# Optimization experiments

Measured on AMD Instinct MI355X. Metric: run time of the kernel, lower is better.

The kernel has to match this reference:

```python
import jax, jax.numpy as jnp
import numpy as np


def setup_inputs() -> dict:
    key = jax.random.key(0)
    ks = jax.random.split(key, 9)
    B, C, H, W = 16, 64, 64, 64
    s = 0.02
    return {
        "x": jax.random.normal(ks[0], (B, C, H, W), dtype=jnp.float32),
        "qw": jax.random.normal(ks[1], (C, C), dtype=jnp.float32) * s,
        "qb": jax.random.normal(ks[2], (C,), dtype=jnp.float32) * s,
        "kw": jax.random.normal(ks[3], (C, C), dtype=jnp.float32) * s,
        "kb": jax.random.normal(ks[4], (C,), dtype=jnp.float32) * s,
        "vw": jax.random.normal(ks[5], (C, C), dtype=jnp.float32) * s,
        "vb": jax.random.normal(ks[6], (C,), dtype=jnp.float32) * s,
        "ow": jax.random.normal(ks[7], (C, C), dtype=jnp.float32) * s,
        "ob": jax.random.normal(ks[8], (C,), dtype=jnp.float32) * s,
    }


def reference(x, qw, qb, kw, kb, vw, vb, ow, ob):
    # x: [B, C, H, W]; 1x1 convs == per-pixel linear maps with weight [out_ch, in_ch]
    B, C, H, W = x.shape
    S = H * W
    xt = x.reshape(B, C, S).transpose(0, 2, 1)  # [B, S, C] tokens over spatial positions
    Q = jnp.einsum("bsc,oc->bso", xt, qw) + qb
    K = jnp.einsum("bsc,oc->bso", xt, kw) + kb
    V = jnp.einsum("bsc,oc->bso", xt, vw) + vb
    scale = 1.0 / jnp.sqrt(jnp.asarray(C, dtype=x.dtype))
    scores = jnp.einsum("bqc,bkc->bqk", Q, K) * scale  # [B, S, S]
    attn = jax.nn.softmax(scores, axis=-1)
    out = jnp.einsum("bqk,bkc->bqc", attn, V)  # [B, S, C]
    out = jnp.einsum("bsc,oc->bso", out, ow) + ob  # out 1x1 conv
    return out.transpose(0, 2, 1).reshape(B, C, H, W)
```

## Files before the change

### kernel.cpp

```cpp
#include <hip/hip_runtime.h>
#include <stdint.h>

#define SS 4096
#define CC 64
#define BB 16

typedef unsigned short u16;
typedef __attribute__((ext_vector_type(8))) __bf16 bf16x8;
typedef __attribute__((ext_vector_type(8))) short short8;
typedef __attribute__((ext_vector_type(4))) float f32x4;

__device__ __forceinline__ uint32_t pkbf(float a, float b) {
    uint32_t ua = __float_as_uint(a) + 0x8000u;
    uint32_t ub = __float_as_uint(b) + 0x8000u;
    return __builtin_amdgcn_perm(ub, ua, 0x07060302u);
}

__device__ __forceinline__ bf16x8 ldw8(const float* p) {
    f32x4 lo = *(const f32x4*)(p);
    f32x4 hi = *(const f32x4*)(p + 4);
    union { uint32_t u[4]; bf16x8 v; } r;
    r.u[0] = pkbf(lo[0], lo[1]);
    r.u[1] = pkbf(lo[2], lo[3]);
    r.u[2] = pkbf(hi[0], hi[1]);
    r.u[3] = pkbf(hi[2], hi[3]);
    return r.v;
}

__global__ __launch_bounds__(256, 4) void qkv_kernel(
    const float* __restrict__ x,
    const float* __restrict__ qw, const float* __restrict__ qb,
    const float* __restrict__ kw, const float* __restrict__ kb,
    const float* __restrict__ vw, const float* __restrict__ vb,
    u16* __restrict__ Q, u16* __restrict__ K, u16* __restrict__ VT)
{
    const int b    = blockIdx.x & 15;
    const int s0   = (blockIdx.x >> 4) << 6;
    const int tid  = threadIdx.x;
    const int w    = tid >> 6;
    const int lane = tid & 63;
    const int lq   = lane & 15;
    const int quad = lane >> 4;

    __shared__ u16 wt[3][64 * 72];
    __shared__ u16 xt[64 * 72];

    for (int m = 0; m < 3; ++m) {
        const float* wsrc = (m == 0) ? qw : ((m == 1) ? kw : vw);
#pragma unroll
        for (int i = 0; i < 8; ++i) {
            int p  = tid + (i << 8);
            int o  = p >> 5;
            int cp = p & 31;
            const float* wp = wsrc + o * 64 + cp * 2;
            ((uint32_t*)&wt[m][o * 72])[cp] = pkbf(wp[0], wp[1]);
        }
    }
    {
        const int sl = tid & 63;
        const int g  = tid >> 6;
        const float* xp = x + (size_t)b * CC * SS + s0 + sl;
#pragma unroll
        for (int i = 0; i < 8; ++i) {
            int p = g + (i << 2);
            float f0 = xp[(size_t)(2 * p) * SS];
            float f1 = xp[(size_t)(2 * p + 1) * SS];
            ((uint32_t*)&xt[sl * 72])[p] = pkbf(f0, f1);
        }
    }
    __syncthreads();

    bf16x8 a0 = *(const bf16x8*)&xt[(w * 16 + lq) * 72 + quad * 8];
    bf16x8 a1 = *(const bf16x8*)&xt[(w * 16 + lq) * 72 + 32 + quad * 8];
    __syncthreads();

    u16* bb = xt + w * (16 * 72);

    const float QSCALE = 0.125f * 1.44269504088896340736f;

    for (int m = 0; m < 3; ++m) {
        const float* bsrc = (m == 0) ? qb : ((m == 1) ? kb : vb);
        bf16x8 bfr[2][4];
#pragma unroll
        for (int kc = 0; kc < 2; ++kc)
#pragma unroll
            for (int nt = 0; nt < 4; ++nt)
                bfr[kc][nt] = *(const bf16x8*)&wt[m][(nt * 16 + lq) * 72 + kc * 32 + quad * 8];

        f32x4 acc[4];
#pragma unroll
        for (int nt = 0; nt < 4; ++nt) {
            float bv = bsrc[nt * 16 + lq];
            acc[nt] = (f32x4){bv, bv, bv, bv};
        }
#pragma unroll
        for (int nt = 0; nt < 4; ++nt) {
            acc[nt] = __builtin_amdgcn_mfma_f32_16x16x32_bf16(a0, bfr[0][nt], acc[nt], 0, 0, 0);
            acc[nt] = __builtin_amdgcn_mfma_f32_16x16x32_bf16(a1, bfr[1][nt], acc[nt], 0, 0, 0);
        }

        if (m == 2) {
#pragma unroll
            for (int nt = 0; nt < 4; ++nt) {
                int c = nt * 16 + lq;
                uint2 pv;
                pv.x = pkbf(acc[nt][0], acc[nt][1]);
                pv.y = pkbf(acc[nt][2], acc[nt][3]);
                *(uint2*)(VT + ((size_t)(b * CC + c)) * SS + s0 + w * 16 + quad * 4) = pv;
            }
        } else {
            const float scl = (m == 0) ? QSCALE : 1.0f;
#pragma unroll
            for (int nt = 0; nt < 4; ++nt)
#pragma unroll
                for (int r = 0; r < 4; ++r)
                    bb[(quad * 4 + r) * 72 + nt * 16 + lq] =
                        (u16)((__float_as_uint(acc[nt][r] * scl) + 0x8000u) >> 16);

            const int row = lane >> 2;
            const int ch  = (lane & 3) << 4;
            short8 v0 = *(const short8*)&bb[row * 72 + ch];
            short8 v1 = *(const short8*)&bb[row * 72 + ch + 8];
            u16* dst = ((m == 0) ? Q : K) + ((size_t)(b * SS + s0 + w * 16 + row)) * CC + ch;
            *(short8*)dst = v0;
            *(short8*)(dst + 8) = v1;
        }
    }
}

__global__ __launch_bounds__(256, 2) void flash_kernel(
    const u16* __restrict__ Q, const u16* __restrict__ K,
    const u16* __restrict__ Vt, const float* __restrict__ ow,
    const float* __restrict__ ob, float* __restrict__ out)
{
    const int b    = blockIdx.x & 15;
    const int q0   = (blockIdx.x >> 4) << 7;
    const int tid  = threadIdx.x;
    const int w    = tid >> 6;
    const int lane = tid & 63;
    const int lq   = lane & 15;
    const int quad = lane >> 4;

    __shared__ u16 lds_k[2][64 * 64];
    __shared__ u16 lds_v[2][64 * 64];
    __shared__ u16 lds_p[8][16 * 64];

    bf16x8 qf[2][2];
#pragma unroll
    for (int g = 0; g < 2; ++g) {
        const u16* qp = Q + ((size_t)(b * SS + q0 + g * 64 + w * 16 + lq)) * CC + quad * 8;
        qf[g][0] = *(const bf16x8*)(qp);
        qf[g][1] = *(const bf16x8*)(qp + 32);
    }

    f32x4 ot[2][4];
#pragma unroll
    for (int g = 0; g < 2; ++g)
#pragma unroll
        for (int ct = 0; ct < 4; ++ct) ot[g][ct] = (f32x4){0.f, 0.f, 0.f, 0.f};
    float lp[2][4] = {{0.f, 0.f, 0.f, 0.f}, {0.f, 0.f, 0.f, 0.f}};

    const int srow = tid >> 2;
    const int a    = tid & 3;
    const u16* kg = K + ((size_t)(b * SS + srow)) * CC + a * 16;
    const u16* vg = Vt + ((size_t)(b * CC + srow)) * SS + a * 16;
    const int sw0 = srow * 64 + (((a << 1)    ) ^ (srow & 7)) * 8;
    const int sw1 = srow * 64 + (((a << 1) | 1) ^ (srow & 7)) * 8;

    {
        short8 k0 = *(const short8*)(kg);
        short8 k1 = *(const short8*)(kg + 8);
        short8 v0 = *(const short8*)(vg);
        short8 v1 = *(const short8*)(vg + 8);
        *(short8*)&lds_k[0][sw0] = k0;
        *(short8*)&lds_k[0][sw1] = k1;
        *(short8*)&lds_v[0][sw0] = v0;
        *(short8*)&lds_v[0][sw1] = v1;
    }

    const int lsw = lq & 7;
    u16* pw0 = lds_p[(w << 1)];
    u16* pw1 = lds_p[(w << 1) | 1];

    for (int kt = 0; kt < 64; ++kt) {
        __syncthreads();
        const int buf = kt & 1;

        const int ktn = (kt + 1) & 63;
        const u16* kgn = kg + (size_t)ktn * (64 * CC);
        const u16* vgn = vg + ktn * 64;
        short8 nk0 = *(const short8*)(kgn);
        short8 nk1 = *(const short8*)(kgn + 8);
        short8 nv0 = *(const short8*)(vgn);
        short8 nv1 = *(const short8*)(vgn + 8);

        bf16x8 kf[2][4];
#pragma unroll
        for (int kc = 0; kc < 2; ++kc)
#pragma unroll
            for (int mt = 0; mt < 4; ++mt)
                kf[kc][mt] = *(const bf16x8*)
                    &lds_k[buf][(mt * 16 + lq) * 64 + (((kc << 2) + quad) ^ lsw) * 8];

        f32x4 sa[2][4];
#pragma unroll
        for (int g = 0; g < 2; ++g)
#pragma unroll
            for (int mt = 0; mt < 4; ++mt) sa[g][mt] = (f32x4){0.f, 0.f, 0.f, 0.f};
#pragma unroll
        for (int g = 0; g < 2; ++g)
#pragma unroll
            for (int kc = 0; kc < 2; ++kc)
#pragma unroll
                for (int mt = 0; mt < 4; ++mt)
                    sa[g][mt] = __builtin_amdgcn_mfma_f32_16x16x32_bf16(
                        kf[kc][mt], qf[g][kc], sa[g][mt], 0, 0, 0);

#pragma unroll
        for (int g = 0; g < 2; ++g) {
            u16* pw = g ? pw1 : pw0;
#pragma unroll
            for (int mt = 0; mt < 4; ++mt) {
                float p0 = __builtin_amdgcn_exp2f(sa[g][mt][0]);
                float p1 = __builtin_amdgcn_exp2f(sa[g][mt][1]);
                float p2 = __builtin_amdgcn_exp2f(sa[g][mt][2]);
                float p3 = __builtin_amdgcn_exp2f(sa[g][mt][3]);
                lp[g][0] += p0; lp[g][1] += p1; lp[g][2] += p2; lp[g][3] += p3;
                uint2 pv;
                pv.x = pkbf(p0, p1);
                pv.y = pkbf(p2, p3);
                *(uint2*)&pw[lq * 64 + (((mt * 2 + (quad >> 1)) ^ lsw) << 3) + (quad & 1) * 4] = pv;
            }
        }

        bf16x8 vf[2][4];
#pragma unroll
        for (int kc = 0; kc < 2; ++kc)
#pragma unroll
            for (int ct = 0; ct < 4; ++ct)
                vf[kc][ct] = *(const bf16x8*)
                    &lds_v[buf][(ct * 16 + lq) * 64 + (((kc << 2) + quad) ^ lsw) * 8];

#pragma unroll
        for (int g = 0; g < 2; ++g) {
            const u16* pw = g ? pw1 : pw0;
#pragma unroll
            for (int kc = 0; kc < 2; ++kc) {
                bf16x8 pf = *(const bf16x8*)
                    &pw[lq * 64 + (((kc * 4 + quad) ^ lsw) << 3)];
#pragma unroll
                for (int ct = 0; ct < 4; ++ct)
                    ot[g][ct] = __builtin_amdgcn_mfma_f32_16x16x32_bf16(
                        vf[kc][ct], pf, ot[g][ct], 0, 0, 0);
            }
        }

        u16* lkd = lds_k[buf ^ 1];
        u16* lvd = lds_v[buf ^ 1];
        *(short8*)&lkd[sw0] = nk0;
        *(short8*)&lkd[sw1] = nk1;
        *(short8*)&lvd[sw0] = nv0;
        *(short8*)&lvd[sw1] = nv1;
    }

    bf16x8 wf[2][4];
#pragma unroll
    for (int kc = 0; kc < 2; ++kc)
#pragma unroll
        for (int nt = 0; nt < 4; ++nt)
            wf[kc][nt] = ldw8(ow + (nt * 16 + lq) * 64 + kc * 32 + quad * 8);
    float bias[4];
#pragma unroll
    for (int nt = 0; nt < 4; ++nt) bias[nt] = ob[nt * 16 + lq];

#pragma unroll
    for (int g = 0; g < 2; ++g) {
        float l = (lp[g][0] + lp[g][1]) + (lp[g][2] + lp[g][3]);
        l += __shfl_xor(l, 16);
        l += __shfl_xor(l, 32);
        const float inv = 1.0f / l;

        u16* po = g ? pw1 : pw0;
#pragma unroll
        for (int ct = 0; ct < 4; ++ct) {
            uint2 pv;
            pv.x = pkbf(ot[g][ct][0] * inv, ot[g][ct][1] * inv);
            pv.y = pkbf(ot[g][ct][2] * inv, ot[g][ct][3] * inv);
            *(uint2*)&po[lq * 64 + (((ct * 2 + (quad >> 1)) ^ lsw) << 3) + (quad & 1) * 4] = pv;
        }
        bf16x8 oa0 = *(const bf16x8*)&po[lq * 64 + (((0 * 4 + quad) ^ lsw) << 3)];
        bf16x8 oa1 = *(const bf16x8*)&po[lq * 64 + (((1 * 4 + quad) ^ lsw) << 3)];

        f32x4 acc[4];
#pragma unroll
        for (int nt = 0; nt < 4; ++nt)
            acc[nt] = (f32x4){bias[nt], bias[nt], bias[nt], bias[nt]};
#pragma unroll
        for (int nt = 0; nt < 4; ++nt) {
            acc[nt] = __builtin_amdgcn_mfma_f32_16x16x32_bf16(oa0, wf[0][nt], acc[nt], 0, 0, 0);
            acc[nt] = __builtin_amdgcn_mfma_f32_16x16x32_bf16(oa1, wf[1][nt], acc[nt], 0, 0, 0);
        }
#pragma unroll
        for (int nt = 0; nt < 4; ++nt) {
            float* dst = out + ((size_t)(b * CC + nt * 16 + lq)) * SS
                       + q0 + g * 64 + w * 16 + quad * 4;
            *(f32x4*)dst = acc[nt];
        }
    }
}

extern "C" void kernel_launch(void* const* d_in, const int* in_sizes, int n_in,
                              void* d_out, int out_size, void* d_ws, size_t ws_size,
                              hipStream_t stream)
{
    const float* x  = (const float*)d_in[0];
    const float* qw = (const float*)d_in[1];
    const float* qb = (const float*)d_in[2];
    const float* kw = (const float*)d_in[3];
    const float* kb = (const float*)d_in[4];
    const float* vw = (const float*)d_in[5];
    const float* vb = (const float*)d_in[6];
    const float* ow = (const float*)d_in[7];
    const float* ob = (const float*)d_in[8];
    float* out = (float*)d_out;

    const size_t T = (size_t)BB * SS * CC;
    u16* Q  = (u16*)d_ws;
    u16* K  = Q + T;
    u16* VT = K + T;

    qkv_kernel<<<dim3(BB * 64), dim3(256), 0, stream>>>(x, qw, qb, kw, kb, vw, vb, Q, K, VT);
    flash_kernel<<<dim3(BB * 32), dim3(256), 0, stream>>>(Q, K, VT, ow, ob, out);
}
```

Measured before the change: 183.1 us.

## Fuse QKV projection into flash kernel via cooperative grid sync

The separate QKV projection launch is merged into the attention kernel. Each block projects its own 128 query rows into LDS, so Q never goes to global memory. Under a cooperative launch each block also computes and writes its slice of K and V^T, then waits at a grid-wide sync before the attention loop. If the cooperative launch fails, a K/V-only projection kernel runs first and the fused kernel then computes only Q. This removes one kernel launch and the Q round trip through memory, but adds a grid barrier and needs all 512 blocks to be resident at once.

```diff
diff --git a/kernel.cpp b/kernel.cpp
--- a/kernel.cpp
+++ b/kernel.cpp
@@ -1,9 +1,12 @@
 #include <hip/hip_runtime.h>
+#include <hip/hip_cooperative_groups.h>
 #include <stdint.h>
 
 #define SS 4096
 #define CC 64
 #define BB 16
+
+namespace cg = cooperative_groups;
 
 typedef unsigned short u16;
 typedef __attribute__((ext_vector_type(8))) __bf16 bf16x8;
@@ -27,12 +30,11 @@
     return r.v;
 }
 
-__global__ __launch_bounds__(256, 4) void qkv_kernel(
+__global__ __launch_bounds__(256, 4) void kv_kernel(
     const float* __restrict__ x,
-    const float* __restrict__ qw, const float* __restrict__ qb,
     const float* __restrict__ kw, const float* __restrict__ kb,
     const float* __restrict__ vw, const float* __restrict__ vb,
-    u16* __restrict__ Q, u16* __restrict__ K, u16* __restrict__ VT)
+    u16* __restrict__ K, u16* __restrict__ VT)
 {
     const int b    = blockIdx.x & 15;
     const int s0   = (blockIdx.x >> 4) << 6;
@@ -42,11 +44,11 @@
     const int lq   = lane & 15;
     const int quad = lane >> 4;
 
-    __shared__ u16 wt[3][64 * 72];
+    __shared__ u16 wt[2][64 * 72];
     __shared__ u16 xt[64 * 72];
 
-    for (int m = 0; m < 3; ++m) {
-        const float* wsrc = (m == 0) ? qw : ((m == 1) ? kw : vw);
+    for (int m = 0; m < 2; ++m) {
+        const float* wsrc = (m == 0) ? kw : vw;
 #pragma unroll
         for (int i = 0; i < 8; ++i) {
             int p  = tid + (i << 8);
@@ -76,10 +78,8 @@
 
     u16* bb = xt + w * (16 * 72);
 
-    const float QSCALE = 0.125f * 1.44269504088896340736f;
-
-    for (int m = 0; m < 3; ++m) {
-        const float* bsrc = (m == 0) ? qb : ((m == 1) ? kb : vb);
+    for (int m = 0; m < 2; ++m) {
+        const float* bsrc = (m == 0) ? kb : vb;
         bf16x8 bfr[2][4];
 #pragma unroll
         for (int kc = 0; kc < 2; ++kc)
@@ -99,7 +99,7 @@
             acc[nt] = __builtin_amdgcn_mfma_f32_16x16x32_bf16(a1, bfr[1][nt], acc[nt], 0, 0, 0);
         }
 
-        if (m == 2) {
+        if (m == 1) {
 #pragma unroll
             for (int nt = 0; nt < 4; ++nt) {
                 int c = nt * 16 + lq;
@@ -109,29 +109,32 @@
                 *(uint2*)(VT + ((size_t)(b * CC + c)) * SS + s0 + w * 16 + quad * 4) = pv;
             }
         } else {
-            const float scl = (m == 0) ? QSCALE : 1.0f;
 #pragma unroll
             for (int nt = 0; nt < 4; ++nt)
 #pragma unroll
                 for (int r = 0; r < 4; ++r)
                     bb[(quad * 4 + r) * 72 + nt * 16 + lq] =
-                        (u16)((__float_as_uint(acc[nt][r] * scl) + 0x8000u) >> 16);
+                        (u16)((__float_as_uint(acc[nt][r]) + 0x8000u) >> 16);
 
             const int row = lane >> 2;
             const int ch  = (lane & 3) << 4;
             short8 v0 = *(const short8*)&bb[row * 72 + ch];
             short8 v1 = *(const short8*)&bb[row * 72 + ch + 8];
-            u16* dst = ((m == 0) ? Q : K) + ((size_t)(b * SS + s0 + w * 16 + row)) * CC + ch;
+            u16* dst = K + ((size_t)(b * SS + s0 + w * 16 + row)) * CC + ch;
             *(short8*)dst = v0;
             *(short8*)(dst + 8) = v1;
         }
     }
 }
 
-__global__ __launch_bounds__(256, 2) void flash_kernel(
-    const u16* __restrict__ Q, const u16* __restrict__ K,
-    const u16* __restrict__ Vt, const float* __restrict__ ow,
-    const float* __restrict__ ob, float* __restrict__ out)
+template <bool COOP>
+__global__ __launch_bounds__(256, 2) void fused_kernel(
+    const float* __restrict__ x,
+    const float* __restrict__ qw, const float* __restrict__ qb,
+    const float* __restrict__ kw, const float* __restrict__ kb,
+    const float* __restrict__ vw, const float* __restrict__ vb,
+    const float* __restrict__ ow, const float* __restrict__ ob,
+    u16* __restrict__ K, u16* __restrict__ VT, float* __restrict__ out)
 {
     const int b    = blockIdx.x & 15;
     const int q0   = (blockIdx.x >> 4) << 7;
@@ -141,17 +144,125 @@
     const int lq   = lane & 15;
     const int quad = lane >> 4;
 
-    __shared__ u16 lds_k[2][64 * 64];
-    __shared__ u16 lds_v[2][64 * 64];
-    __shared__ u16 lds_p[8][16 * 64];
+    __shared__ u16 smem[24576];
+    u16* WT = smem;
+    u16* XT = smem + 13824;
+
+    const int NW = COOP ? 3 : 1;
+    for (int m = 0; m < NW; ++m) {
+        const float* wsrc = COOP ? ((m == 0) ? vw : ((m == 1) ? kw : qw)) : qw;
+#pragma unroll
+        for (int i = 0; i < 8; ++i) {
+            int p  = tid + (i << 8);
+            int o  = p >> 5;
+            int cp = p & 31;
+            const float* wp = wsrc + o * 64 + cp * 2;
+            ((uint32_t*)&WT[m * 4608 + o * 72])[cp] = pkbf(wp[0], wp[1]);
+        }
+    }
+    {
+        const int sl = tid & 127;
+        const int g  = tid >> 7;
+        const float* xp = x + (size_t)b * CC * SS + q0 + sl;
+#pragma unroll
+        for (int i = 0; i < 16; ++i) {
+            int p = g + (i << 1);
+            float f0 = xp[(size_t)(2 * p) * SS];
+            float f1 = xp[(size_t)(2 * p + 1) * SS];
+            ((uint32_t*)&XT[sl * 72])[p] = pkbf(f0, f1);
+        }
+    }
+    __syncthreads();
+
+    bf16x8 af[2][2];
+#pragma unroll
+    for (int mt = 0; mt < 2; ++mt) {
+        const int srow = w * 32 + mt * 16;
+        af[mt][0] = *(const bf16x8*)&XT[(srow + lq) * 72 + quad * 8];
+        af[mt][1] = *(const bf16x8*)&XT[(srow + lq) * 72 + 32 + quad * 8];
+    }
+
+    const float QSCALE = 0.125f * 1.44269504088896340736f;
+
+    for (int m = 0; m < NW; ++m) {
+        const float* bsrc = COOP ? ((m == 0) ? vb : ((m == 1) ? kb : qb)) : qb;
+        const u16* wm = WT + m * 4608;
+        bf16x8 bfr[2][4];
+#pragma unroll
+        for (int kc = 0; kc < 2; ++kc)
+#pragma unroll
+            for (int nt = 0; nt < 4; ++nt)
+                bfr[kc][nt] = *(const bf16x8*)&wm[(nt * 16 + lq) * 72 + kc * 32 + quad * 8];
+
+#pragma unroll
+        for (int mt = 0; mt < 2; ++mt) {
+            const int srow = w * 32 + mt * 16;
+            f32x4 acc[4];
+#pragma unroll
+            for (int nt = 0; nt < 4; ++nt) {
+                float bv = bsrc[nt * 16 + lq];
+                acc[nt] = (f32x4){bv, bv, bv, bv};
+            }
+#pragma unroll
+            for (int nt = 0; nt < 4; ++nt) {
+                acc[nt] = __builtin_amdgcn_mfma_f32_16x16x32_bf16(af[mt][0], bfr[0][nt], acc[nt], 0, 0, 0);
+                acc[nt] = __builtin_amdgcn_mfma_f32_16x16x32_bf16(af[mt][1], bfr[1][nt], acc[nt], 0, 0, 0);
+            }
+
+            if (COOP && m == 0) {
+#pragma unroll
+                for (int nt = 0; nt < 4; ++nt) {
+                    int c = nt * 16 + lq;
+                    uint2 pv;
+                    pv.x = pkbf(acc[nt][0], acc[nt][1]);
+                    pv.y = pkbf(acc[nt][2], acc[nt][3]);
+                    *(uint2*)(VT + ((size_t)(b * CC + c)) * SS + q0 + srow + quad * 4) = pv;
+                }
+            } else if (COOP && m == 1) {
+                u16* bb = XT + srow * 72;
+#pragma unroll
+                for (int nt = 0; nt < 4; ++nt)
+#pragma unroll
+                    for (int r = 0; r < 4; ++r)
+                        bb[(quad * 4 + r) * 72 + nt * 16 + lq] =
+                            (u16)((__float_as_uint(acc[nt][r]) + 0x8000u) >> 16);
+
+                const int row = lane >> 2;
+                const int ch  = (lane & 3) << 4;
+                short8 v0 = *(const short8*)&bb[row * 72 + ch];
+                short8 v1 = *(const short8*)&bb[row * 72 + ch + 8];
+                u16* dst = K + ((size_t)(b * SS + q0 + srow + row)) * CC + ch;
+                *(short8*)dst = v0;
+                *(short8*)(dst + 8) = v1;
+            } else {
+#pragma unroll
+                for (int nt = 0; nt < 4; ++nt)
+#pragma unroll
+                    for (int r = 0; r < 4; ++r)
+                        XT[(srow + quad * 4 + r) * 72 + nt * 16 + lq] =
+                            (u16)((__float_as_uint(acc[nt][r] * QSCALE) + 0x8000u) >> 16);
+            }
+        }
+    }
+    __syncthreads();
 
     bf16x8 qf[2][2];
 #pragma unroll
     for (int g = 0; g < 2; ++g) {
-        const u16* qp = Q + ((size_t)(b * SS + q0 + g * 64 + w * 16 + lq)) * CC + quad * 8;
-        qf[g][0] = *(const bf16x8*)(qp);
-        qf[g][1] = *(const bf16x8*)(qp + 32);
-    }
+        const int row = g * 64 + w * 16 + lq;
+        qf[g][0] = *(const bf16x8*)&XT[row * 72 + quad * 8];
+        qf[g][1] = *(const bf16x8*)&XT[row * 72 + 32 + quad * 8];
+    }
+
+    if constexpr (COOP) {
+        cg::this_grid().sync();
+    } else {
+        __syncthreads();
+    }
+
+    u16* lds_k = smem;
+    u16* lds_v = smem + 8192;
+    u16* lds_p = smem + 16384;
 
     f32x4 ot[2][4];
 #pragma unroll
@@ -163,7 +274,7 @@
     const int srow = tid >> 2;
     const int a    = tid & 3;
     const u16* kg = K + ((size_t)(b * SS + srow)) * CC + a * 16;
-    const u16* vg = Vt + ((size_t)(b * CC + srow)) * SS + a * 16;
+    const u16* vg = VT + ((size_t)(b * CC + srow)) * SS + a * 16;
     const int sw0 = srow * 64 + (((a << 1)    ) ^ (srow & 7)) * 8;
     const int sw1 = srow * 64 + (((a << 1) | 1) ^ (srow & 7)) * 8;
 
@@ -172,19 +283,19 @@
         short8 k1 = *(const short8*)(kg + 8);
         short8 v0 = *(const short8*)(vg);
         short8 v1 = *(const short8*)(vg + 8);
-        *(short8*)&lds_k[0][sw0] = k0;
-        *(short8*)&lds_k[0][sw1] = k1;
-        *(short8*)&lds_v[0][sw0] = v0;
-        *(short8*)&lds_v[0][sw1] = v1;
+        *(short8*)&lds_k[sw0] = k0;
+        *(short8*)&lds_k[sw1] = k1;
+        *(short8*)&lds_v[sw0] = v0;
+        *(short8*)&lds_v[sw1] = v1;
     }
 
     const int lsw = lq & 7;
-    u16* pw0 = lds_p[(w << 1)];
-    u16* pw1 = lds_p[(w << 1) | 1];
+    u16* pw0 = lds_p + (w << 1) * 1024;
+    u16* pw1 = pw0 + 1024;
 
     for (int kt = 0; kt < 64; ++kt) {
         __syncthreads();
-        const int buf = kt & 1;
+        const int bo = (kt & 1) << 12;
 
         const int ktn = (kt + 1) & 63;
         const u16* kgn = kg + (size_t)ktn * (64 * CC);
@@ -200,7 +311,7 @@
 #pragma unroll
             for (int mt = 0; mt < 4; ++mt)
                 kf[kc][mt] = *(const bf16x8*)
-                    &lds_k[buf][(mt * 16 + lq) * 64 + (((kc << 2) + quad) ^ lsw) * 8];
+                    &lds_k[bo + (mt * 16 + lq) * 64 + (((kc << 2) + quad) ^ lsw) * 8];
 
         f32x4 sa[2][4];
 #pragma unroll
@@ -239,7 +350,7 @@
 #pragma unroll
             for (int ct = 0; ct < 4; ++ct)
                 vf[kc][ct] = *(const bf16x8*)
-                    &lds_v[buf][(ct * 16 + lq) * 64 + (((kc << 2) + quad) ^ lsw) * 8];
+                    &lds_v[bo + (ct * 16 + lq) * 64 + (((kc << 2) + quad) ^ lsw) * 8];
 
 #pragma unroll
         for (int g = 0; g < 2; ++g) {
@@ -255,12 +366,11 @@
             }
         }
 
-        u16* lkd = lds_k[buf ^ 1];
-        u16* lvd = lds_v[buf ^ 1];
-        *(short8*)&lkd[sw0] = nk0;
-        *(short8*)&lkd[sw1] = nk1;
-        *(short8*)&lvd[sw0] = nv0;
-        *(short8*)&lvd[sw1] = nv1;
+        const int bn = 4096 - bo;
+        *(short8*)&lds_k[bn + sw0] = nk0;
+        *(short8*)&lds_k[bn + sw1] = nk1;
+        *(short8*)&lds_v[bn + sw0] = nv0;
+        *(short8*)&lds_v[bn + sw1] = nv1;
     }
 
     bf16x8 wf[2][4];
@@ -325,10 +435,19 @@
     float* out = (float*)d_out;
 
     const size_t T = (size_t)BB * SS * CC;
-    u16* Q  = (u16*)d_ws;
-    u16* K  = Q + T;
+    u16* K  = (u16*)d_ws;
     u16* VT = K + T;
 
-    qkv_kernel<<<dim3(BB * 64), dim3(256), 0, stream>>>(x, qw, qb, kw, kb, vw, vb, Q, K, VT);
-    flash_kernel<<<dim3(BB * 32), dim3(256), 0, stream>>>(Q, K, VT, ow, ob, out);
+    void* args[] = {(void*)&x, (void*)&qw, (void*)&qb, (void*)&kw, (void*)&kb,
+                    (void*)&vw, (void*)&vb, (void*)&ow, (void*)&ob,
+                    (void*)&K, (void*)&VT, (void*)&out};
+    hipError_t e = hipLaunchCooperativeKernel((void*)&fused_kernel<true>,
+                                              dim3(BB * 32), dim3(256),
+                                              args, 0, stream);
+    if (e != hipSuccess) {
+        (void)hipGetLastError();
+        kv_kernel<<<dim3(BB * 64), dim3(256), 0, stream>>>(x, kw, kb, vw, vb, K, VT);
+        fused_kernel<false><<<dim3(BB * 32), dim3(256), 0, stream>>>(
+            x, qw, qb, kw, kb, vw, vb, ow, ob, K, VT, out);
+    }
 }
```

Measured after the change: 257.4 us. 1.41x slower.
